# Kernel tuning notes

Hardware: AMD Instinct MI355X
Metric: run time of the kernel (lower is better)

Reference implementation:

```python
import jax, jax.numpy as jnp
import numpy as np

B, S, H, I, E, K = 4, 2048, 1024, 4096, 8, 2


def setup_inputs() -> dict:
    key = jax.random.key(0)
    ks = jax.random.split(key, 6)
    x = jax.random.normal(ks[0], (B, S, H), dtype=jnp.float32)
    gate_w = jax.random.normal(ks[1], (H, E), dtype=jnp.float32) * 0.02
    up_w = jax.random.normal(ks[2], (E, H, I), dtype=jnp.float32) * 0.02
    up_b = jnp.zeros((E, I), dtype=jnp.float32)
    down_w = jax.random.normal(ks[3], (E, I, H), dtype=jnp.float32) * 0.02
    down_b = jnp.zeros((E, H), dtype=jnp.float32)
    return {"x": x, "gate_w": gate_w, "up_w": up_w, "up_b": up_b,
            "down_w": down_w, "down_b": down_b}


def reference(x, gate_w, up_w, up_b, down_w, down_b):
    # Router: logits [B,S,E], softmax probs
    logits = jnp.einsum('bsh,he->bse', x, gate_w)
    probs = jax.nn.softmax(logits, axis=-1)
    # top-k selection and renormalization of the selected probabilities
    topk_p, topk_idx = jax.lax.top_k(probs, K)            # [B,S,K]
    topk_p = topk_p / jnp.sum(topk_p, axis=-1, keepdims=True)
    # combine weights per expert: [B,S,E] (sum of renormalized top-k probs routed to e)
    combine = jnp.sum(jax.nn.one_hot(topk_idx, E, dtype=x.dtype) * topk_p[..., None], axis=2)
    # per-expert FFN, weighted combine (loop over fixed small expert set)
    out = jnp.zeros_like(x)
    for e in range(E):
        h = jax.nn.gelu(jnp.einsum('bsh,hi->bsi', x, up_w[e]) + up_b[e], approximate=False)
        y = jnp.einsum('bsi,ih->bsh', h, down_w[e]) + down_b[e]
        out = out + combine[..., e:e + 1] * y
    # aux statistics
    expert_usage = jnp.mean(probs, axis=(0, 1))           # [E]
    load_balance_loss = E * jnp.sum(expert_usage * expert_usage)
    top_expert = topk_idx[..., 0]                          # [B,S]
    return out, load_balance_loss, expert_usage, top_expert
```

## Files before the change

### kernel.cpp

```cpp
#include <hip/hip_runtime.h>
#include <cmath>

#define T_TOK 8192
#define HDIM 1024
#define IDIM 4096
#define NEXP 8

#define OFF_LOSS  8388608
#define OFF_USAGE 8388609
#define OFF_TOPE  8388617

typedef __attribute__((ext_vector_type(8))) short bf16x8;
typedef __attribute__((ext_vector_type(4))) float f32x4;
typedef unsigned short u16;
typedef unsigned int u32;

__device__ inline u16 f2bf(float f) {
  u32 u = __float_as_uint(f);
  u32 r = (u + 0x7FFFu + ((u >> 16) & 1u)) >> 16;
  return (u16)r;
}

__device__ inline void glds16(const void* g, void* l) {
  __builtin_amdgcn_global_load_lds(
      (const __attribute__((address_space(1))) u32*)g,
      (__attribute__((address_space(3))) u32*)l, 16, 0, 0);
}

__global__ __launch_bounds__(256)
void cvt_x(const float* __restrict__ x, u16* __restrict__ xb) {
  size_t i = ((size_t)blockIdx.x * 256 + threadIdx.x) * 8;
  float4 a = *(const float4*)(x + i);
  float4 b = *(const float4*)(x + i + 4);
  union { u16 s[8]; uint4 v; } u;
  u.s[0] = f2bf(a.x); u.s[1] = f2bf(a.y); u.s[2] = f2bf(a.z); u.s[3] = f2bf(a.w);
  u.s[4] = f2bf(b.x); u.s[5] = f2bf(b.y); u.s[6] = f2bf(b.z); u.s[7] = f2bf(b.w);
  *(uint4*)(xb + i) = u.v;
}

__global__ __launch_bounds__(256)
void transpose_cvt(const float* __restrict__ src, u16* __restrict__ dst, int R, int C) {
  __shared__ float tile[32][33];
  size_t eoff = (size_t)blockIdx.z * R * C;
  int r0 = blockIdx.y * 32, c0 = blockIdx.x * 32;
  int tx = threadIdx.x & 31, ty = threadIdx.x >> 5;
  const float* s = src + eoff;
  u16* d = dst + eoff;
#pragma unroll
  for (int k = 0; k < 4; k++)
    tile[ty + 8*k][tx] = s[(size_t)(r0 + ty + 8*k) * C + c0 + tx];
  __syncthreads();
#pragma unroll
  for (int k = 0; k < 4; k++)
    d[(size_t)(c0 + ty + 8*k) * R + r0 + tx] = f2bf(tile[tx][ty + 8*k]);
}

__global__ __launch_bounds__(64)
void router_kernel(const float* __restrict__ x, const float* __restrict__ gw,
                   float* __restrict__ probs, int* __restrict__ counts,
                   int* __restrict__ tlist, float* __restrict__ wlist,
                   float* __restrict__ out) {
  int tok = blockIdx.x;
  int lane = threadIdx.x;
  double acc[NEXP];
#pragma unroll
  for (int e = 0; e < NEXP; e++) acc[e] = 0.0;
  const float* xr = x + (size_t)tok * HDIM;
  for (int h = lane; h < HDIM; h += 64) {
    double xv = (double)xr[h];
    const float* g = gw + h * NEXP;
#pragma unroll
    for (int e = 0; e < NEXP; e++) acc[e] += xv * (double)g[e];
  }
#pragma unroll
  for (int off = 32; off > 0; off >>= 1) {
#pragma unroll
    for (int e = 0; e < NEXP; e++) acc[e] += __shfl_xor(acc[e], off);
  }
  if (lane == 0) {
    double m = acc[0];
#pragma unroll
    for (int e = 1; e < NEXP; e++) if (acc[e] > m) m = acc[e];
    double p[NEXP], ssum = 0.0;
#pragma unroll
    for (int e = 0; e < NEXP; e++) { p[e] = exp(acc[e] - m); ssum += p[e]; }
#pragma unroll
    for (int e = 0; e < NEXP; e++) p[e] /= ssum;
    int i1 = 0;
#pragma unroll
    for (int e = 1; e < NEXP; e++) if (p[e] > p[i1]) i1 = e;
    int i2 = (i1 == 0) ? 1 : 0;
#pragma unroll
    for (int e = 0; e < NEXP; e++) if (e != i1 && p[e] > p[i2]) i2 = e;
    double ps = p[i1] + p[i2];
#pragma unroll
    for (int e = 0; e < NEXP; e++) probs[(size_t)tok * NEXP + e] = (float)p[e];
    out[OFF_TOPE + tok] = (float)i1;
    int pos1 = atomicAdd(&counts[i1], 1);
    tlist[i1 * T_TOK + pos1] = tok;
    wlist[i1 * T_TOK + pos1] = (float)(p[i1] / ps);
    int pos2 = atomicAdd(&counts[i2], 1);
    tlist[i2 * T_TOK + pos2] = tok;
    wlist[i2 * T_TOK + pos2] = (float)(p[i2] / ps);
  }
}

__global__ void hbase_kernel(const int* __restrict__ counts, int* __restrict__ hbase) {
  if (threadIdx.x == 0 && blockIdx.x == 0) {
    int s = 0;
    for (int e = 0; e < NEXP; e++) { hbase[e] = s; s += counts[e]; }
    hbase[NEXP] = s;
  }
}

__global__ __launch_bounds__(256)
void usage_kernel(const float* __restrict__ probs, float* __restrict__ out) {
  int e = blockIdx.x;
  float s = 0.f;
  for (int t = threadIdx.x; t < T_TOK; t += 256) s += probs[(size_t)t * NEXP + e];
#pragma unroll
  for (int off = 32; off > 0; off >>= 1) s += __shfl_xor(s, off);
  __shared__ float red[4];
  int lane = threadIdx.x & 63, wid = threadIdx.x >> 6;
  if (lane == 0) red[wid] = s;
  __syncthreads();
  if (threadIdx.x == 0)
    out[OFF_USAGE + e] = (red[0] + red[1] + red[2] + red[3]) / (float)T_TOK;
}

__global__ void loss_kernel(float* __restrict__ out) {
  if (threadIdx.x == 0 && blockIdx.x == 0) {
    float s = 0.f;
    for (int e = 0; e < NEXP; e++) { float u = out[OFF_USAGE + e]; s += u * u; }
    out[OFF_LOSS] = (float)NEXP * s;
  }
}


__global__ __launch_bounds__(256, 3)
void up_gemm(const u16* __restrict__ xb, const u16* __restrict__ wbt,
             const float* __restrict__ bias, const int* __restrict__ counts,
             const int* __restrict__ hbase, const int* __restrict__ tlist,
             u16* __restrict__ hout, int e_fixed) {
  const int NT = IDIM / 128;
  const int MT = T_TOK / 128;
  int q = gridDim.x >> 3;
  int orig = blockIdx.x;
  int wg = (orig & 7) * q + (orig >> 3);
  int e, tm, tn;
  if (e_fixed >= 0) { e = e_fixed; tm = wg / NT; tn = wg % NT; }
  else { e = wg / (MT * NT); int r = wg % (MT * NT); tm = r / NT; tn = r % NT; }
  int cnt = counts[e];
  int m0 = tm * 128;
  if (m0 >= cnt) return;
  int hb = (e_fixed >= 0) ? 0 : hbase[e];
  int n0 = tn * 128;

  __shared__ u16 As[2 * 4096];
  __shared__ u16 Bs[2 * 4096];

  int t = threadIdx.x;
  int ra = t >> 2;
  int sw = (t & 3) ^ ((ra >> 1) & 3);

  const int* tl = tlist + e * T_TOK;
  int g0 = m0 + ra;      if (g0 > cnt - 1) g0 = cnt - 1;
  int g1 = m0 + ra + 64; if (g1 > cnt - 1) g1 = cnt - 1;
  const u16* pa0 = xb + (size_t)tl[g0] * HDIM + sw * 8;
  const u16* pa1 = xb + (size_t)tl[g1] * HDIM + sw * 8;
  const u16* wb = wbt + (size_t)e * IDIM * HDIM;
  const u16* pb0 = wb + (size_t)(n0 + ra) * HDIM + sw * 8;
  const u16* pb1 = wb + (size_t)(n0 + ra + 64) * HDIM + sw * 8;

  f32x4 acc[4][4];
#pragma unroll
  for (int i = 0; i < 4; i++)
#pragma unroll
    for (int j = 0; j < 4; j++) acc[i][j] = (f32x4){0.f, 0.f, 0.f, 0.f};

  int lane = t & 63, wid = t >> 6;
  int wr = (wid >> 1) * 64, wc = (wid & 1) * 64;
  int lrow = lane & 15, lslot = lane >> 4;

  auto stage = [&](int b, int k0) {
    u16* a = &As[b * 4096];
    u16* bb = &Bs[b * 4096];
    glds16(pa0 + k0, a + t * 8);
    glds16(pa1 + k0, a + 2048 + t * 8);
    glds16(pb0 + k0, bb + t * 8);
    glds16(pb1 + k0, bb + 2048 + t * 8);
  };
  auto compute = [&](int b) {
    const u16* A = &As[b * 4096];
    const u16* Bb = &Bs[b * 4096];
    bf16x8 af[4], bfv[4];
#pragma unroll
    for (int mi = 0; mi < 4; mi++) {
      int row = wr + mi * 16 + lrow;
      af[mi] = *(const bf16x8*)&A[row * 32 + ((lslot ^ ((row >> 1) & 3)) * 8)];
    }
#pragma unroll
    for (int ni = 0; ni < 4; ni++) {
      int row = wc + ni * 16 + lrow;
      bfv[ni] = *(const bf16x8*)&Bb[row * 32 + ((lslot ^ ((row >> 1) & 3)) * 8)];
    }
#pragma unroll
    for (int mi = 0; mi < 4; mi++)
#pragma unroll
      for (int ni = 0; ni < 4; ni++)
        acc[mi][ni] = __builtin_amdgcn_mfma_f32_16x16x32_bf16(af[mi], bfv[ni], acc[mi][ni], 0, 0, 0);
  };

  const int nk = HDIM / 32;
  stage(0, 0);
  for (int kt = 0; kt < nk; ++kt) {
    int b = kt & 1;
    __builtin_amdgcn_s_barrier();
    if (kt + 1 < nk) {
      stage(b ^ 1, (kt + 1) * 32);
      asm volatile("s_waitcnt vmcnt(4)" ::: "memory");
    } else {
      asm volatile("s_waitcnt vmcnt(0)" ::: "memory");
    }
    compute(b);
  }

  float bv[4];
#pragma unroll
  for (int ni = 0; ni < 4; ni++)
    bv[ni] = bias[(size_t)e * IDIM + n0 + wc + ni * 16 + lrow];
  int r4 = lslot * 4;
#pragma unroll
  for (int mi = 0; mi < 4; mi++) {
    int rb = m0 + wr + mi * 16 + r4;
#pragma unroll
    for (int j = 0; j < 4; j++) {
      int row = rb + j;
      if (row < cnt) {
        u16* hp = hout + (size_t)(hb + row) * IDIM + n0 + wc + lrow;
#pragma unroll
        for (int ni = 0; ni < 4; ni++) {
          float v = acc[mi][ni][j] + bv[ni];
          float gl = 0.5f * v * (1.0f + erff(v * 0.70710678118654752f));
          hp[ni * 16] = f2bf(gl);
        }
      }
    }
  }
}

__global__ __launch_bounds__(256, 3)
void down_gemm(const u16* __restrict__ h, const u16* __restrict__ wbt,
               const float* __restrict__ bias, const int* __restrict__ counts,
               const int* __restrict__ hbase, const int* __restrict__ tlist,
               const float* __restrict__ wlist, float* __restrict__ out, int e_fixed) {
  const int NT = HDIM / 128;
  const int MT = T_TOK / 128;
  int q = gridDim.x >> 3;
  int orig = blockIdx.x;
  int wg = (orig & 7) * q + (orig >> 3);
  int e, tm, tn;
  if (e_fixed >= 0) { e = e_fixed; tm = wg / NT; tn = wg % NT; }
  else { e = wg / (MT * NT); int r = wg % (MT * NT); tm = r / NT; tn = r % NT; }
  int cnt = counts[e];
  int m0 = tm * 128;
  if (m0 >= cnt) return;
  int hb = (e_fixed >= 0) ? 0 : hbase[e];
  int n0 = tn * 128;

  __shared__ u16 As[2 * 4096];
  __shared__ u16 Bs[2 * 4096];

  int t = threadIdx.x;
  int ra = t >> 2;
  int sw = (t & 3) ^ ((ra >> 1) & 3);

  int g0 = m0 + ra;      if (g0 > cnt - 1) g0 = cnt - 1;
  int g1 = m0 + ra + 64; if (g1 > cnt - 1) g1 = cnt - 1;
  const u16* pa0 = h + (size_t)(hb + g0) * IDIM + sw * 8;
  const u16* pa1 = h + (size_t)(hb + g1) * IDIM + sw * 8;
  const u16* wb = wbt + (size_t)e * HDIM * IDIM;
  const u16* pb0 = wb + (size_t)(n0 + ra) * IDIM + sw * 8;
  const u16* pb1 = wb + (size_t)(n0 + ra + 64) * IDIM + sw * 8;

  f32x4 acc[4][4];
#pragma unroll
  for (int i = 0; i < 4; i++)
#pragma unroll
    for (int j = 0; j < 4; j++) acc[i][j] = (f32x4){0.f, 0.f, 0.f, 0.f};

  int lane = t & 63, wid = t >> 6;
  int wr = (wid >> 1) * 64, wc = (wid & 1) * 64;
  int lrow = lane & 15, lslot = lane >> 4;

  auto stage = [&](int b, int k0) {
    u16* a = &As[b * 4096];
    u16* bb = &Bs[b * 4096];
    glds16(pa0 + k0, a + t * 8);
    glds16(pa1 + k0, a + 2048 + t * 8);
    glds16(pb0 + k0, bb + t * 8);
    glds16(pb1 + k0, bb + 2048 + t * 8);
  };
  auto compute = [&](int b) {
    const u16* A = &As[b * 4096];
    const u16* Bb = &Bs[b * 4096];
    bf16x8 af[4], bfv[4];
#pragma unroll
    for (int mi = 0; mi < 4; mi++) {
      int row = wr + mi * 16 + lrow;
      af[mi] = *(const bf16x8*)&A[row * 32 + ((lslot ^ ((row >> 1) & 3)) * 8)];
    }
#pragma unroll
    for (int ni = 0; ni < 4; ni++) {
      int row = wc + ni * 16 + lrow;
      bfv[ni] = *(const bf16x8*)&Bb[row * 32 + ((lslot ^ ((row >> 1) & 3)) * 8)];
    }
#pragma unroll
    for (int mi = 0; mi < 4; mi++)
#pragma unroll
      for (int ni = 0; ni < 4; ni++)
        acc[mi][ni] = __builtin_amdgcn_mfma_f32_16x16x32_bf16(af[mi], bfv[ni], acc[mi][ni], 0, 0, 0);
  };

  const int nk = IDIM / 32;
  stage(0, 0);
  for (int kt = 0; kt < nk; ++kt) {
    int b = kt & 1;
    __builtin_amdgcn_s_barrier();
    if (kt + 1 < nk) {
      stage(b ^ 1, (kt + 1) * 32);
      asm volatile("s_waitcnt vmcnt(4)" ::: "memory");
    } else {
      asm volatile("s_waitcnt vmcnt(0)" ::: "memory");
    }
    compute(b);
  }

  float bv[4];
#pragma unroll
  for (int ni = 0; ni < 4; ni++)
    bv[ni] = bias[(size_t)e * HDIM + n0 + wc + ni * 16 + lrow];
  int r4 = lslot * 4;
#pragma unroll
  for (int mi = 0; mi < 4; mi++) {
    int rb = m0 + wr + mi * 16 + r4;
#pragma unroll
    for (int j = 0; j < 4; j++) {
      int row = rb + j;
      if (row < cnt) {
        int tok = tlist[e * T_TOK + row];
        float w = wlist[e * T_TOK + row];
        float* op = out + (size_t)tok * HDIM + n0 + wc + lrow;
#pragma unroll
        for (int ni = 0; ni < 4; ni++)
          atomicAdd(&op[ni * 16], w * (acc[mi][ni][j] + bv[ni]));
      }
    }
  }
}

extern "C" void kernel_launch(void* const* d_in, const int* in_sizes, int n_in,
                              void* d_out, int out_size, void* d_ws, size_t ws_size,
                              hipStream_t stream) {
  const float* x   = (const float*)d_in[0];
  const float* gw  = (const float*)d_in[1];
  const float* upw = (const float*)d_in[2];
  const float* upb = (const float*)d_in[3];
  const float* dnw = (const float*)d_in[4];
  const float* dnb = (const float*)d_in[5];
  float* out = (float*)d_out;
  char* ws = (char*)d_ws;

  int*   counts = (int*)(ws + 0);
  int*   hbase  = (int*)(ws + 64);
  int*   tlist  = (int*)(ws + 256);
  float* wlist  = (float*)(ws + 256 + 262144);
  float* probs  = (float*)(ws + 256 + 2 * 262144);
  u16*   xb     = (u16*)(ws + 1048576);
  u16*   upbt   = (u16*)(ws + 1048576 + 16777216);
  u16*   dnbt   = (u16*)(ws + 1048576 + 16777216 + 67108864ull);
  u16*   hbuf   = (u16*)(ws + 1048576 + 16777216 + 2ull * 67108864ull);

  bool grouped = ws_size >= 286261248ull;

  hipMemsetAsync(counts, 0, 32, stream);
  hipMemsetAsync(d_out, 0, (size_t)out_size * 4, stream);

  cvt_x<<<4096, 256, 0, stream>>>(x, xb);
  transpose_cvt<<<dim3(IDIM / 32, HDIM / 32, NEXP), 256, 0, stream>>>(upw, upbt, HDIM, IDIM);
  transpose_cvt<<<dim3(HDIM / 32, IDIM / 32, NEXP), 256, 0, stream>>>(dnw, dnbt, IDIM, HDIM);
  router_kernel<<<T_TOK, 64, 0, stream>>>(x, gw, probs, counts, tlist, wlist, out);
  hbase_kernel<<<1, 64, 0, stream>>>(counts, hbase);
  usage_kernel<<<NEXP, 256, 0, stream>>>(probs, out);
  loss_kernel<<<1, 64, 0, stream>>>(out);

  if (grouped) {
    up_gemm<<<NEXP * 64 * 32, 256, 0, stream>>>(xb, upbt, upb, counts, hbase, tlist, hbuf, -1);
    down_gemm<<<NEXP * 64 * 8, 256, 0, stream>>>(hbuf, dnbt, dnb, counts, hbase, tlist, wlist, out, -1);
  } else {
    for (int e = 0; e < NEXP; e++) {
      up_gemm<<<64 * 32, 256, 0, stream>>>(xb, upbt, upb, counts, hbase, tlist, hbuf, e);
      down_gemm<<<64 * 8, 256, 0, stream>>>(hbuf, dnbt, dnb, counts, hbase, tlist, wlist, out, e);
    }
  }
}
```

Measured before the change: 794.1 us.

## Split-K down GEMM, widen transpose tiles, pack router tokens per block

The down-projection GEMM is split into two K halves, each accumulating into the output with atomics and the bias applied only by the first half. This doubles the number of workgroups so the GPU stays occupied when experts hold few tokens. The weight transpose now uses 64x64 tiles with float4 loads and 16-byte bf16 stores, and the router packs four tokens per 256-thread block. The split-K change doubles the atomic traffic to the output and makes floating-point summation order nondeterministic.

Result: faster. 768.0 us (-3.3%).

```diff
diff --git a/kernel.cpp b/kernel.cpp
--- a/kernel.cpp
+++ b/kernel.cpp
@@ -39,29 +39,41 @@
 }
 
 __global__ __launch_bounds__(256)
-void transpose_cvt(const float* __restrict__ src, u16* __restrict__ dst, int R, int C) {
-  __shared__ float tile[32][33];
+void transpose_cvt64(const float* __restrict__ src, u16* __restrict__ dst, int R, int C) {
+  __shared__ float tile[64][65];
   size_t eoff = (size_t)blockIdx.z * R * C;
-  int r0 = blockIdx.y * 32, c0 = blockIdx.x * 32;
-  int tx = threadIdx.x & 31, ty = threadIdx.x >> 5;
+  int r0 = blockIdx.y * 64, c0 = blockIdx.x * 64;
   const float* s = src + eoff;
   u16* d = dst + eoff;
-#pragma unroll
-  for (int k = 0; k < 4; k++)
-    tile[ty + 8*k][tx] = s[(size_t)(r0 + ty + 8*k) * C + c0 + tx];
+  int tr = threadIdx.x >> 4;
+  int tc = (threadIdx.x & 15) * 4;
+#pragma unroll
+  for (int it = 0; it < 4; it++) {
+    int row = tr + it * 16;
+    float4 v = *(const float4*)(s + (size_t)(r0 + row) * C + c0 + tc);
+    tile[row][tc] = v.x; tile[row][tc + 1] = v.y;
+    tile[row][tc + 2] = v.z; tile[row][tc + 3] = v.w;
+  }
   __syncthreads();
-#pragma unroll
-  for (int k = 0; k < 4; k++)
-    d[(size_t)(c0 + ty + 8*k) * R + r0 + tx] = f2bf(tile[tx][ty + 8*k]);
-}
-
-__global__ __launch_bounds__(64)
+  int wc = threadIdx.x >> 3;
+  int wr = (threadIdx.x & 7) * 8;
+#pragma unroll
+  for (int it = 0; it < 2; it++) {
+    int c = wc + it * 32;
+    union { u16 s[8]; uint4 v; } u;
+#pragma unroll
+    for (int j = 0; j < 8; j++) u.s[j] = f2bf(tile[wr + j][c]);
+    *(uint4*)(d + (size_t)(c0 + c) * R + r0 + wr) = u.v;
+  }
+}
+
+__global__ __launch_bounds__(256)
 void router_kernel(const float* __restrict__ x, const float* __restrict__ gw,
                    float* __restrict__ probs, int* __restrict__ counts,
                    int* __restrict__ tlist, float* __restrict__ wlist,
                    float* __restrict__ out) {
-  int tok = blockIdx.x;
-  int lane = threadIdx.x;
+  int wid = threadIdx.x >> 6, lane = threadIdx.x & 63;
+  int tok = blockIdx.x * 4 + wid;
   double acc[NEXP];
 #pragma unroll
   for (int e = 0; e < NEXP; e++) acc[e] = 0.0;
@@ -256,17 +268,23 @@
                const float* __restrict__ wlist, float* __restrict__ out, int e_fixed) {
   const int NT = HDIM / 128;
   const int MT = T_TOK / 128;
+  const int KS = 2;
   int q = gridDim.x >> 3;
   int orig = blockIdx.x;
   int wg = (orig & 7) * q + (orig >> 3);
-  int e, tm, tn;
-  if (e_fixed >= 0) { e = e_fixed; tm = wg / NT; tn = wg % NT; }
-  else { e = wg / (MT * NT); int r = wg % (MT * NT); tm = r / NT; tn = r % NT; }
+  int e, r;
+  if (e_fixed >= 0) { e = e_fixed; r = wg; }
+  else { e = wg / (MT * NT * KS); r = wg % (MT * NT * KS); }
+  int tm = r / (NT * KS);
+  int r2 = r % (NT * KS);
+  int ks = r2 / NT;
+  int tn = r2 % NT;
   int cnt = counts[e];
   int m0 = tm * 128;
   if (m0 >= cnt) return;
   int hb = (e_fixed >= 0) ? 0 : hbase[e];
   int n0 = tn * 128;
+  int kbase = ks * (IDIM / KS);
 
   __shared__ u16 As[2 * 4096];
   __shared__ u16 Bs[2 * 4096];
@@ -322,13 +340,13 @@
         acc[mi][ni] = __builtin_amdgcn_mfma_f32_16x16x32_bf16(af[mi], bfv[ni], acc[mi][ni], 0, 0, 0);
   };
 
-  const int nk = IDIM / 32;
-  stage(0, 0);
+  const int nk = (IDIM / KS) / 32;
+  stage(0, kbase);
   for (int kt = 0; kt < nk; ++kt) {
     int b = kt & 1;
     __builtin_amdgcn_s_barrier();
     if (kt + 1 < nk) {
-      stage(b ^ 1, (kt + 1) * 32);
+      stage(b ^ 1, kbase + (kt + 1) * 32);
       asm volatile("s_waitcnt vmcnt(4)" ::: "memory");
     } else {
       asm volatile("s_waitcnt vmcnt(0)" ::: "memory");
@@ -339,7 +357,7 @@
   float bv[4];
 #pragma unroll
   for (int ni = 0; ni < 4; ni++)
-    bv[ni] = bias[(size_t)e * HDIM + n0 + wc + ni * 16 + lrow];
+    bv[ni] = (ks == 0) ? bias[(size_t)e * HDIM + n0 + wc + ni * 16 + lrow] : 0.0f;
   int r4 = lslot * 4;
 #pragma unroll
   for (int mi = 0; mi < 4; mi++) {
@@ -387,20 +405,20 @@
   hipMemsetAsync(d_out, 0, (size_t)out_size * 4, stream);
 
   cvt_x<<<4096, 256, 0, stream>>>(x, xb);
-  transpose_cvt<<<dim3(IDIM / 32, HDIM / 32, NEXP), 256, 0, stream>>>(upw, upbt, HDIM, IDIM);
-  transpose_cvt<<<dim3(HDIM / 32, IDIM / 32, NEXP), 256, 0, stream>>>(dnw, dnbt, IDIM, HDIM);
-  router_kernel<<<T_TOK, 64, 0, stream>>>(x, gw, probs, counts, tlist, wlist, out);
+  transpose_cvt64<<<dim3(IDIM / 64, HDIM / 64, NEXP), 256, 0, stream>>>(upw, upbt, HDIM, IDIM);
+  transpose_cvt64<<<dim3(HDIM / 64, IDIM / 64, NEXP), 256, 0, stream>>>(dnw, dnbt, IDIM, HDIM);
+  router_kernel<<<T_TOK / 4, 256, 0, stream>>>(x, gw, probs, counts, tlist, wlist, out);
   hbase_kernel<<<1, 64, 0, stream>>>(counts, hbase);
   usage_kernel<<<NEXP, 256, 0, stream>>>(probs, out);
   loss_kernel<<<1, 64, 0, stream>>>(out);
 
   if (grouped) {
     up_gemm<<<NEXP * 64 * 32, 256, 0, stream>>>(xb, upbt, upb, counts, hbase, tlist, hbuf, -1);
-    down_gemm<<<NEXP * 64 * 8, 256, 0, stream>>>(hbuf, dnbt, dnb, counts, hbase, tlist, wlist, out, -1);
+    down_gemm<<<NEXP * 64 * 8 * 2, 256, 0, stream>>>(hbuf, dnbt, dnb, counts, hbase, tlist, wlist, out, -1);
   } else {
     for (int e = 0; e < NEXP; e++) {
       up_gemm<<<64 * 32, 256, 0, stream>>>(xb, upbt, upb, counts, hbase, tlist, hbuf, e);
-      down_gemm<<<64 * 8, 256, 0, stream>>>(hbuf, dnbt, dnb, counts, hbase, tlist, wlist, out, e);
-    }
-  }
-}
+      down_gemm<<<64 * 8 * 2, 256, 0, stream>>>(hbuf, dnbt, dnb, counts, hbase, tlist, wlist, out, e);
+    }
+  }
+}
```
